# Kernel optimization log

Hardware: AMD Instinct MI355X
Metric: run time of the kernel (lower is better)

## Reference

```python
import jax, jax.numpy as jnp
import numpy as np

EPS = 1e-5

def _sparse_conv(x, nbr, W):
    # x: [N, Cin], nbr: [N, K] indices into rows of x, W: [K, Cin, Cout]
    # Minkowski-style kernel-map conv: gather neighbor feats, contract per offset.
    return jnp.einsum('nkc,kcd->nd', x[nbr], W)

def _bn(x, gamma, beta):
    # BatchNorm over all points (training-mode, biased variance)
    mu = x.mean(axis=0)
    var = x.var(axis=0)
    return (x - mu) * jax.lax.rsqrt(var + EPS) * gamma + beta

def setup_inputs() -> dict:
    key = jax.random.key(0)
    ks = jax.random.split(key, 6)
    N, K, Cin, Cout = 100000, 27, 64, 128
    x = jax.random.normal(ks[0], (N, Cin), dtype=jnp.float32)
    nbr = jax.random.randint(ks[1], (N, K), 0, N, dtype=jnp.int64)
    W1 = jax.random.normal(ks[2], (K, Cin, Cout), dtype=jnp.float32) / np.sqrt(K * Cin)
    W2 = jax.random.normal(ks[3], (K, Cout, Cout), dtype=jnp.float32) / np.sqrt(K * Cout)
    Wd = jax.random.normal(ks[4], (Cin, Cout), dtype=jnp.float32) / np.sqrt(Cin)
    ones = jnp.ones((Cout,), jnp.float32)
    zeros = jnp.zeros((Cout,), jnp.float32)
    return {"x": x, "nbr": nbr, "W1": W1, "g1": ones, "b1": zeros,
            "W2": W2, "g2": ones, "b2": zeros, "Wd": Wd, "gd": ones, "bd": zeros}

def reference(x, nbr, W1, g1, b1, W2, g2, b2, Wd, gd, bd):
    h = jax.nn.relu(_bn(_sparse_conv(x, nbr, W1), g1, b1))
    h = jax.nn.relu(_bn(_sparse_conv(h, nbr, W2), g2, b2))
    # downsample branch (input_nc != output_nc): 1x1 sparse conv == matmul, + BN
    res = _bn(x @ Wd, gd, bd)
    return h + res
```

## Files before the change

### kernel.cpp

```cpp
#include <hip/hip_runtime.h>
#include <hip/hip_bf16.h>

typedef unsigned short u16;
typedef unsigned int   u32;

#define COUT 128
#define KNB  27

typedef __attribute__((ext_vector_type(8))) __bf16 bf16x8;
typedef __attribute__((ext_vector_type(4))) float  f32x4;

__device__ float g_sum[2][128], g_sq[2][128];
__device__ float g_colsum[64], g_G[4096];
__device__ float g_sc[3][128], g_sh[3][128];
__device__ int   g_f32;
__device__ int   g_i64;
__device__ __attribute__((aligned(16))) u16 g_W1t[KNB * 128 * 64];
__device__ __attribute__((aligned(16))) u16 g_W2t[KNB * 128 * 128];

__device__ __forceinline__ float b2f(u32 u) {
    union { float f; u32 i; } v; v.i = u << 16; return v.f;
}
__device__ __forceinline__ u16 f2b(float f) {
    union { float f; u32 i; } v; v.f = f;
    u32 r = v.i + 0x7fffu + ((v.i >> 16) & 1u);
    return (u16)(r >> 16);
}
__device__ __forceinline__ float ldf(const void* p, int i, bool f32) {
    return f32 ? ((const float*)p)[i] : b2f((u32)((const u16*)p)[i]);
}

__device__ __forceinline__ void gld16(const void* g, void* l) {
    __builtin_amdgcn_global_load_lds(
        (const __attribute__((address_space(1))) u32*)g,
        (__attribute__((address_space(3))) u32*)l, 16, 0, 0);
}

__device__ __forceinline__ void lds_sync() {
    asm volatile("s_waitcnt lgkmcnt(0)" ::: "memory");
    __builtin_amdgcn_s_barrier();
    asm volatile("" ::: "memory");
}

__global__ void probe_zero_kernel(const u16* __restrict__ g1w, const int* __restrict__ nbr)
{
    int t = threadIdx.x;
    if (t == 0) {
        g_f32 = (g1w[0] == 0) ? 1 : 0;
        g_i64 = ((nbr[1] | nbr[3] | nbr[5] | nbr[7]) == 0) ? 1 : 0;
    }
    for (int i = t; i < 128; i += 256) {
        g_sum[0][i] = 0.f; g_sq[0][i] = 0.f;
        g_sum[1][i] = 0.f; g_sq[1][i] = 0.f;
    }
    for (int i = t; i < 64; i += 256) g_colsum[i] = 0.f;
    for (int i = t; i < 4096; i += 256) g_G[i] = 0.f;
}

__global__ void convert_w_kernel(const void* __restrict__ W1, const void* __restrict__ W2,
                                 const void* __restrict__ x, u16* __restrict__ xb, int N)
{
    const bool f32 = (g_f32 != 0);
    const int total1 = KNB * 64 * 128;
    const int total2 = KNB * 128 * 128;
    const int stride = gridDim.x * 256;
    for (int e = blockIdx.x * 256 + threadIdx.x; e < total1 + total2; e += stride) {
        if (e < total1) {
            int k = e / (64 * 128), r = e % (64 * 128);
            int c = r / 128, d = r % 128;
            g_W1t[(k * 128 + d) * 64 + c] = f2b(ldf(W1, e, f32));
        } else {
            int e2 = e - total1;
            int k = e2 / (128 * 128), r = e2 % (128 * 128);
            int c = r / 128, d = r % 128;
            g_W2t[(k * 128 + d) * 128 + c] = f2b(ldf(W2, e2, f32));
        }
    }
    const int totalx4 = (N * 64) / 4;
    for (int e = blockIdx.x * 256 + threadIdx.x; e < totalx4; e += stride) {
        if (f32) {
            float4 v = ((const float4*)x)[e];
            ushort4 r;
            r.x = f2b(v.x); r.y = f2b(v.y); r.z = f2b(v.z); r.w = f2b(v.w);
            ((ushort4*)xb)[e] = r;
        } else {
            ((uint2*)xb)[e] = ((const uint2*)x)[e];
        }
    }
}

__global__ __launch_bounds__(256)
void bn_relu_kernel(u16* __restrict__ tmp, int N)
{
    const int t  = threadIdx.x;
    const int c0 = (t & 15) * 8;
    float sc[8], sh[8];
#pragma unroll
    for (int j = 0; j < 8; ++j) { sc[j] = g_sc[0][c0 + j]; sh[j] = g_sh[0][c0 + j]; }
    const int total = N * (COUT / 8);
    for (int e = blockIdx.x * 256 + t; e < total; e += gridDim.x * 256) {
        uint4 u = ((const uint4*)tmp)[e];
        float v[8] = { b2f(u.x & 0xffffu), b2f(u.x >> 16),
                       b2f(u.y & 0xffffu), b2f(u.y >> 16),
                       b2f(u.z & 0xffffu), b2f(u.z >> 16),
                       b2f(u.w & 0xffffu), b2f(u.w >> 16) };
#pragma unroll
        for (int j = 0; j < 8; ++j) v[j] = fmaxf(fmaf(v[j], sc[j], sh[j]), 0.f);
        uint4 o;
        o.x = (u32)f2b(v[0]) | ((u32)f2b(v[1]) << 16);
        o.y = (u32)f2b(v[2]) | ((u32)f2b(v[3]) << 16);
        o.z = (u32)f2b(v[4]) | ((u32)f2b(v[5]) << 16);
        o.w = (u32)f2b(v[6]) | ((u32)f2b(v[7]) << 16);
        ((uint4*)tmp)[e] = o;
    }
}

template<int CIN, bool OUTF32, int WSEL, int SSEL>
__global__ __launch_bounds__(256, 2)
void spconv_mfma(const u16* __restrict__ src, const int* __restrict__ nbr,
                 void* __restrict__ outv, int N)
{
    constexpr int NCHUNK = CIN / 64;
    constexpr int STEPS  = KNB * NCHUNK;
    constexpr int OFF_ODD = (NCHUNK == 2) ? 64 : 0;
    const u16* __restrict__ Wt = (WSEL == 1) ? g_W1t : g_W2t;

    __shared__ __attribute__((aligned(16))) u16 As[2 * 8192];
    __shared__ __attribute__((aligned(16))) u16 Bs[2 * 8192];

    const int t    = threadIdx.x;
    const int lane = t & 63;
    const int w    = t >> 6;
    const int m    = lane & 15;
    const int q4   = lane >> 4;
    const int s_st = w >> 1;
    const int par  = w & 1;
    const int wm   = w >> 1;
    const int wn   = w & 1;
    const int n0   = blockIdx.x * 128;
    const int coff = (s_st * 4 + q4) * 8;
    const int kst  = (g_i64 != 0) ? 2 : 1;

    u32 nb0[4];
#pragma unroll
    for (int i = 0; i < 4; ++i) {
        int gr  = n0 + (2 * i + par) * 16 + m;
        int grc = (gr < N) ? gr : (N - 1);
        nb0[i] = (u32)grc * (u32)(KNB * kst);
    }

    f32x4 acc[4][4];
#pragma unroll
    for (int a = 0; a < 4; ++a)
#pragma unroll
        for (int b = 0; b < 4; ++b) acc[a][b] = (f32x4){0.f, 0.f, 0.f, 0.f};

    int idxE[4], idxO[4];

#define STEP_K(S)  ((NCHUNK == 2) ? ((S) >> 1) : (S))
#define LOAD_IDX(DST, K) do { \
    int kk_ = (K) < KNB ? (K) : (KNB - 1); \
    _Pragma("unroll") \
    for (int i_ = 0; i_ < 4; ++i_) \
        DST[i_] = nbr[nb0[i_] + (u32)kk_ * (u32)kst]; \
} while (0)

#define ISSUE_STEP(BUFO, IDX, K, C0N) do { \
    _Pragma("unroll") \
    for (int i_ = 0; i_ < 4; ++i_) { \
        const int tile_ = 2 * i_ + par; \
        u32 rw_ = (u32)(IDX)[i_]; if (rw_ >= (u32)N) rw_ = 0; \
        gld16(src + (size_t)rw_ * CIN + (C0N) + coff, \
              &As[(BUFO) + (tile_ * 2 + s_st) * 512]); \
        gld16(Wt + ((size_t)(K) * 128 + tile_ * 16 + m) * CIN + (C0N) + coff, \
              &Bs[(BUFO) + (tile_ * 2 + s_st) * 512]); \
    } \
} while (0)

#define MFMA_PHASE(LOFS) do { \
    __builtin_amdgcn_s_setprio(1); \
    _Pragma("unroll") \
    for (int s2_ = 0; s2_ < 2; ++s2_) { \
        bf16x8 afr_[4]; \
        _Pragma("unroll") \
        for (int mt_ = 0; mt_ < 4; ++mt_) \
            afr_[mt_] = *(const bf16x8*)&As[(LOFS) + (((wm * 4 + mt_) * 2 + s2_) * 512) + lane * 8]; \
        _Pragma("unroll") \
        for (int nt_ = 0; nt_ < 4; ++nt_) { \
            bf16x8 bfr_ = *(const bf16x8*)&Bs[(LOFS) + (((wn * 4 + nt_) * 2 + s2_) * 512) + lane * 8]; \
            _Pragma("unroll") \
            for (int mt_ = 0; mt_ < 4; ++mt_) \
                acc[mt_][nt_] = __builtin_amdgcn_mfma_f32_16x16x32_bf16( \
                    afr_[mt_], bfr_, acc[mt_][nt_], 0, 0, 0); \
        } \
    } \
    __builtin_amdgcn_s_setprio(0); \
} while (0)

    LOAD_IDX(idxE, 0);
    LOAD_IDX(idxO, STEP_K(1));
    ISSUE_STEP(0, idxE, 0, 0);
    LOAD_IDX(idxE, STEP_K(2));

#pragma clang loop unroll(disable)
    for (int s = 0; s < STEPS; s += 2) {
        lds_sync();
        if (s + 1 < STEPS) {
            ISSUE_STEP(8192, idxO, STEP_K(s + 1), OFF_ODD);
            LOAD_IDX(idxO, STEP_K(s + 3));
            asm volatile("s_waitcnt vmcnt(16)" ::: "memory");
        } else {
            asm volatile("s_waitcnt vmcnt(0)" ::: "memory");
        }
        __builtin_amdgcn_s_barrier();
        asm volatile("" ::: "memory");
        MFMA_PHASE(0);

        if (s + 1 < STEPS) {
            lds_sync();
            if (s + 2 < STEPS) {
                ISSUE_STEP(0, idxE, STEP_K(s + 2), 0);
                LOAD_IDX(idxE, STEP_K(s + 4));
                asm volatile("s_waitcnt vmcnt(16)" ::: "memory");
            } else {
                asm volatile("s_waitcnt vmcnt(0)" ::: "memory");
            }
            __builtin_amdgcn_s_barrier();
            asm volatile("" ::: "memory");
            MFMA_PHASE(8192);
        }
    }

    const int qq = lane >> 4, nn = lane & 15;
#pragma unroll
    for (int mt = 0; mt < 4; ++mt) {
#pragma unroll
        for (int r4 = 0; r4 < 4; ++r4) {
            int gr = n0 + (wm * 4 + mt) * 16 + qq * 4 + r4;
            if (gr < N) {
#pragma unroll
                for (int nt = 0; nt < 4; ++nt) {
                    float val = acc[mt][nt][r4];
                    size_t off = (size_t)gr * COUT + (wn * 4 + nt) * 16 + nn;
                    if constexpr (OUTF32) ((float*)outv)[off] = val;
                    else                  ((u16*)outv)[off]   = f2b(val);
                }
            }
        }
    }

    if constexpr (SSEL >= 0) {
        float sS[4], sQ[4];
#pragma unroll
        for (int nt = 0; nt < 4; ++nt) { sS[nt] = 0.f; sQ[nt] = 0.f; }
#pragma unroll
        for (int mt = 0; mt < 4; ++mt) {
#pragma unroll
            for (int r4 = 0; r4 < 4; ++r4) {
                int gr = n0 + (wm * 4 + mt) * 16 + qq * 4 + r4;
                bool ok = (gr < N);
#pragma unroll
                for (int nt = 0; nt < 4; ++nt) {
                    float v = ok ? acc[mt][nt][r4] : 0.f;
                    sS[nt] += v;
                    sQ[nt] = fmaf(v, v, sQ[nt]);
                }
            }
        }
#pragma unroll
        for (int nt = 0; nt < 4; ++nt) {
            sS[nt] += __shfl_xor(sS[nt], 16);
            sS[nt] += __shfl_xor(sS[nt], 32);
            sQ[nt] += __shfl_xor(sQ[nt], 16);
            sQ[nt] += __shfl_xor(sQ[nt], 32);
        }
        lds_sync();
        float* red = (float*)As;
        if (lane < 16) {
#pragma unroll
            for (int nt = 0; nt < 4; ++nt) {
                red[w * 64 + nt * 16 + lane]       = sS[nt];
                red[256 + w * 64 + nt * 16 + lane] = sQ[nt];
            }
        }
        lds_sync();
        if (t < 128) {
            int hi = t >> 6, lo = t & 63;
            float S = red[hi * 64 + lo] + red[(hi + 2) * 64 + lo];
            float Q = red[256 + hi * 64 + lo] + red[256 + (hi + 2) * 64 + lo];
            atomicAdd(&g_sum[SSEL][t], S);
            atomicAdd(&g_sq[SSEL][t],  Q);
        }
    }
#undef STEP_K
#undef LOAD_IDX
#undef ISSUE_STEP
#undef MFMA_PHASE
}

template<int SEL>
__global__ void finalize_kernel(const void* __restrict__ g, const void* __restrict__ b,
                                float invN)
{
    const bool f32 = (g_f32 != 0);
    int c = threadIdx.x;
    float mu  = g_sum[SEL][c] * invN;
    float var = fmaxf(g_sq[SEL][c] * invN - mu * mu, 0.f);
    float rs  = rsqrtf(var + 1e-5f);
    float sc  = rs * ldf(g, c, f32);
    g_sc[SEL][c] = sc;
    g_sh[SEL][c] = ldf(b, c, f32) - mu * sc;
}

__global__ __launch_bounds__(256)
void xstats_kernel(const void* __restrict__ xv, int N)
{
    __shared__ float xs[16 * 64];
    const bool f32 = (g_f32 != 0);
    const int t  = threadIdx.x;
    const int c  = t >> 2;
    const int cb = (t & 3) * 16;
    float acc[16];
#pragma unroll
    for (int j = 0; j < 16; ++j) acc[j] = 0.f;
    float cs = 0.f;

    for (int r0 = blockIdx.x * 16; r0 < N; r0 += gridDim.x * 16) {
        __syncthreads();
        {
            int e = t * 4;
            int rr = e >> 6, qq = e & 63;
            int row = r0 + rr;
            size_t off = (size_t)min(row, N - 1) * 64 + qq;
            bool ok = (row < N);
            float v0, v1, v2, v3;
            if (f32) {
                float4 vv = *(const float4*)((const float*)xv + off);
                v0 = vv.x; v1 = vv.y; v2 = vv.z; v3 = vv.w;
            } else {
                uint2 u = *(const uint2*)((const u16*)xv + off);
                v0 = b2f(u.x & 0xffffu); v1 = b2f(u.x >> 16);
                v2 = b2f(u.y & 0xffffu); v3 = b2f(u.y >> 16);
            }
            xs[e + 0] = ok ? v0 : 0.f;
            xs[e + 1] = ok ? v1 : 0.f;
            xs[e + 2] = ok ? v2 : 0.f;
            xs[e + 3] = ok ? v3 : 0.f;
        }
        __syncthreads();
#pragma unroll
        for (int rr = 0; rr < 16; ++rr) {
            float a = xs[rr * 64 + c];
#pragma unroll
            for (int j = 0; j < 16; ++j)
                acc[j] = fmaf(a, xs[rr * 64 + cb + j], acc[j]);
        }
        if (t < 64) {
#pragma unroll
            for (int rr = 0; rr < 16; ++rr) cs += xs[rr * 64 + t];
        }
    }
#pragma unroll
    for (int j = 0; j < 16; ++j) atomicAdd(&g_G[c * 64 + cb + j], acc[j]);
    if (t < 64) atomicAdd(&g_colsum[t], cs);
}

__global__ __launch_bounds__(128)
void finalize_d_kernel(const void* __restrict__ Wd, const void* __restrict__ gd,
                       const void* __restrict__ bd, float invN)
{
    __shared__ float Gs[64 * 64];
    const bool f32 = (g_f32 != 0);
    const int t = threadIdx.x;
    for (int e = t; e < 4096; e += 128) Gs[e] = g_G[e];
    __syncthreads();
    float w[64];
#pragma unroll
    for (int c = 0; c < 64; ++c) w[c] = ldf(Wd, c * 128 + t, f32);
    float s = 0.f, q = 0.f;
    for (int c = 0; c < 64; ++c) {
        float inner = 0.f;
#pragma unroll 8
        for (int cc = 0; cc < 64; ++cc) inner = fmaf(Gs[c * 64 + cc], w[cc], inner);
        q = fmaf(w[c], inner, q);
        s = fmaf(g_colsum[c], w[c], s);
    }
    float mu  = s * invN;
    float var = fmaxf(q * invN - mu * mu, 0.f);
    float rs  = rsqrtf(var + 1e-5f);
    float sc  = rs * ldf(gd, t, f32);
    g_sc[2][t] = sc;
    g_sh[2][t] = ldf(bd, t, f32) - mu * sc;
}

__global__ __launch_bounds__(256)
void finish_dense_kernel(const void* __restrict__ xv, const void* __restrict__ Wdv,
                         float* __restrict__ out, int N)
{
    __shared__ float Xs[64 * 68];
    __shared__ float Ws[64 * COUT];
    const bool f32 = (g_f32 != 0);
    const int t  = threadIdx.x;
    const int tx = t & 31;
    const int ty = t >> 5;
    const int n0 = blockIdx.x * 64;
    const int valid = min(64, N - n0);

    for (int e = t; e < 64 * 16; e += 256) {
        int mm = e >> 4;
        int qq = (e & 15) << 2;
        size_t off = (size_t)min(n0 + mm, N - 1) * 64 + qq;
        float v0, v1, v2, v3;
        if (f32) {
            float4 vv = *(const float4*)((const float*)xv + off);
            v0 = vv.x; v1 = vv.y; v2 = vv.z; v3 = vv.w;
        } else {
            uint2 u = *(const uint2*)((const u16*)xv + off);
            v0 = b2f(u.x & 0xffffu); v1 = b2f(u.x >> 16);
            v2 = b2f(u.y & 0xffffu); v3 = b2f(u.y >> 16);
        }
        *(float4*)&Xs[mm * 68 + qq] = make_float4(v0, v1, v2, v3);
    }
    if (f32) {
        const float* Wp = (const float*)Wdv;
        for (int e = t; e < (64 * COUT) / 8; e += 256) {
            int l = e << 3;
            float4 a = *(const float4*)(Wp + l);
            float4 b = *(const float4*)(Wp + l + 4);
            float* dst = &Ws[l];
            dst[0]=a.x; dst[1]=a.y; dst[2]=a.z; dst[3]=a.w;
            dst[4]=b.x; dst[5]=b.y; dst[6]=b.z; dst[7]=b.w;
        }
    } else {
        const u16* Wp = (const u16*)Wdv;
        for (int e = t; e < (64 * COUT) / 8; e += 256) {
            int l = e << 3;
            uint4 u = *(const uint4*)(Wp + l);
            float* dst = &Ws[l];
            dst[0] = b2f(u.x & 0xffffu); dst[1] = b2f(u.x >> 16);
            dst[2] = b2f(u.y & 0xffffu); dst[3] = b2f(u.y >> 16);
            dst[4] = b2f(u.z & 0xffffu); dst[5] = b2f(u.z >> 16);
            dst[6] = b2f(u.w & 0xffffu); dst[7] = b2f(u.w >> 16);
        }
    }
    __syncthreads();

    float acc[8][4];
#pragma unroll
    for (int mm = 0; mm < 8; ++mm)
#pragma unroll
        for (int j = 0; j < 4; ++j) acc[mm][j] = 0.f;

#pragma unroll 2
    for (int c = 0; c < 64; ++c) {
        float4 wv = *(const float4*)&Ws[c * COUT + tx * 4];
#pragma unroll
        for (int mm = 0; mm < 8; ++mm) {
            float a = Xs[(ty * 8 + mm) * 68 + c];
            acc[mm][0] = fmaf(a, wv.x, acc[mm][0]);
            acc[mm][1] = fmaf(a, wv.y, acc[mm][1]);
            acc[mm][2] = fmaf(a, wv.z, acc[mm][2]);
            acc[mm][3] = fmaf(a, wv.w, acc[mm][3]);
        }
    }

    const int d = tx * 4;
    float s2r[4] = {g_sc[1][d], g_sc[1][d+1], g_sc[1][d+2], g_sc[1][d+3]};
    float h2r[4] = {g_sh[1][d], g_sh[1][d+1], g_sh[1][d+2], g_sh[1][d+3]};
    float sdr[4] = {g_sc[2][d], g_sc[2][d+1], g_sc[2][d+2], g_sc[2][d+3]};
    float hdr[4] = {g_sh[2][d], g_sh[2][d+1], g_sh[2][d+2], g_sh[2][d+3]};
#pragma unroll
    for (int mm = 0; mm < 8; ++mm) {
        int rr = ty * 8 + mm;
        if (rr < valid) {
            float* p = out + (size_t)(n0 + rr) * COUT + d;
            float4 raw = *(float4*)p;
            float o0 = fmaxf(fmaf(raw.x, s2r[0], h2r[0]), 0.f) + fmaf(acc[mm][0], sdr[0], hdr[0]);
            float o1 = fmaxf(fmaf(raw.y, s2r[1], h2r[1]), 0.f) + fmaf(acc[mm][1], sdr[1], hdr[1]);
            float o2 = fmaxf(fmaf(raw.z, s2r[2], h2r[2]), 0.f) + fmaf(acc[mm][2], sdr[2], hdr[2]);
            float o3 = fmaxf(fmaf(raw.w, s2r[3], h2r[3]), 0.f) + fmaf(acc[mm][3], sdr[3], hdr[3]);
            *(float4*)p = make_float4(o0, o1, o2, o3);
        }
    }
}

extern "C" void kernel_launch(void* const* d_in, const int* in_sizes, int n_in,
                              void* d_out, int out_size, void* d_ws, size_t ws_size,
                              hipStream_t stream)
{
    const void* x   = d_in[0];
    const int*  nbr = (const int*)d_in[1];
    const void* W1  = d_in[2];
    const void* g1  = d_in[3];
    const void* b1  = d_in[4];
    const void* W2  = d_in[5];
    const void* g2  = d_in[6];
    const void* b2  = d_in[7];
    const void* Wd  = d_in[8];
    const void* gd  = d_in[9];
    const void* bd  = d_in[10];
    float* out = (float*)d_out;

    const int N = in_sizes[0] / 64;
    u16* tmp = (u16*)d_ws;
    u16* xb  = (u16*)d_out;

    const int nbm = (N + 127) / 128;
    const int nbf = (N + 63) / 64;
    const float invN = 1.f / (float)N;

    hipLaunchKernelGGL(probe_zero_kernel, dim3(1), dim3(256), 0, stream,
                       (const u16*)g1, nbr);
    hipLaunchKernelGGL(convert_w_kernel, dim3(1024), dim3(256), 0, stream,
                       W1, W2, x, xb, N);
    hipLaunchKernelGGL((spconv_mfma<64, false, 1, 0>), dim3(nbm), dim3(256), 0, stream,
                       xb, nbr, tmp, N);
    hipLaunchKernelGGL((finalize_kernel<0>), dim3(1), dim3(128), 0, stream, g1, b1, invN);
    hipLaunchKernelGGL(bn_relu_kernel, dim3(2048), dim3(256), 0, stream, tmp, N);
    hipLaunchKernelGGL((spconv_mfma<128, true, 2, 1>), dim3(nbm), dim3(256), 0, stream,
                       tmp, nbr, out, N);
    hipLaunchKernelGGL((finalize_kernel<1>), dim3(1), dim3(128), 0, stream, g2, b2, invN);
    hipLaunchKernelGGL(xstats_kernel, dim3(256), dim3(256), 0, stream, x, N);
    hipLaunchKernelGGL(finalize_d_kernel, dim3(1), dim3(128), 0, stream, Wd, gd, bd, invN);
    hipLaunchKernelGGL(finish_dense_kernel, dim3(nbf), dim3(256), 0, stream,
                       x, Wd, out, N);
}
```

Before: 811.7 us.

## Halve K-chunk to 32 channels to cut LDS and raise occupancy to four blocks

The sparse-conv MFMA kernel now stages 32-channel chunks per step instead of 64, halving the A/B LDS double buffers. Launch bounds rise to four blocks per CU, and each step issues fewer gathers with adjusted vmcnt waits. The aim is more resident waves to hide the latency of random neighbor gathers. In exchange there are twice as many pipeline steps and barriers, each with less MFMA work, and a tighter register budget that could spill.

After: 827.7 us. Within noise of the previous version (+2.0%).

```diff
diff --git a/kernel.cpp b/kernel.cpp
--- a/kernel.cpp
+++ b/kernel.cpp
@@ -116,35 +116,31 @@
 }
 
 template<int CIN, bool OUTF32, int WSEL, int SSEL>
-__global__ __launch_bounds__(256, 2)
+__global__ __launch_bounds__(256, 4)
 void spconv_mfma(const u16* __restrict__ src, const int* __restrict__ nbr,
                  void* __restrict__ outv, int N)
 {
-    constexpr int NCHUNK = CIN / 64;
-    constexpr int STEPS  = KNB * NCHUNK;
-    constexpr int OFF_ODD = (NCHUNK == 2) ? 64 : 0;
+    constexpr int CHUNKS = CIN / 32;
+    constexpr int STEPS  = KNB * CHUNKS;
     const u16* __restrict__ Wt = (WSEL == 1) ? g_W1t : g_W2t;
 
-    __shared__ __attribute__((aligned(16))) u16 As[2 * 8192];
-    __shared__ __attribute__((aligned(16))) u16 Bs[2 * 8192];
+    __shared__ __attribute__((aligned(16))) u16 As[2 * 4096];
+    __shared__ __attribute__((aligned(16))) u16 Bs[2 * 4096];
 
     const int t    = threadIdx.x;
     const int lane = t & 63;
     const int w    = t >> 6;
     const int m    = lane & 15;
     const int q4   = lane >> 4;
-    const int s_st = w >> 1;
-    const int par  = w & 1;
     const int wm   = w >> 1;
     const int wn   = w & 1;
     const int n0   = blockIdx.x * 128;
-    const int coff = (s_st * 4 + q4) * 8;
     const int kst  = (g_i64 != 0) ? 2 : 1;
 
-    u32 nb0[4];
-#pragma unroll
-    for (int i = 0; i < 4; ++i) {
-        int gr  = n0 + (2 * i + par) * 16 + m;
+    u32 nb0[2];
+#pragma unroll
+    for (int i = 0; i < 2; ++i) {
+        int gr  = n0 + (w + 4 * i) * 16 + m;
         int grc = (gr < N) ? gr : (N - 1);
         nb0[i] = (u32)grc * (u32)(KNB * kst);
     }
@@ -155,44 +151,41 @@
 #pragma unroll
         for (int b = 0; b < 4; ++b) acc[a][b] = (f32x4){0.f, 0.f, 0.f, 0.f};
 
-    int idxE[4], idxO[4];
-
-#define STEP_K(S)  ((NCHUNK == 2) ? ((S) >> 1) : (S))
+    int idxE[2], idxO[2];
+
+#define STEP_K(S)  ((S) / CHUNKS)
 #define LOAD_IDX(DST, K) do { \
     int kk_ = (K) < KNB ? (K) : (KNB - 1); \
+    DST[0] = nbr[nb0[0] + (u32)kk_ * (u32)kst]; \
+    DST[1] = nbr[nb0[1] + (u32)kk_ * (u32)kst]; \
+} while (0)
+
+#define ISSUE_STEP(BUFO, IDX, K, S) do { \
+    const int cb_ = ((S) & (CHUNKS - 1)) * 32; \
     _Pragma("unroll") \
-    for (int i_ = 0; i_ < 4; ++i_) \
-        DST[i_] = nbr[nb0[i_] + (u32)kk_ * (u32)kst]; \
-} while (0)
-
-#define ISSUE_STEP(BUFO, IDX, K, C0N) do { \
-    _Pragma("unroll") \
-    for (int i_ = 0; i_ < 4; ++i_) { \
-        const int tile_ = 2 * i_ + par; \
+    for (int i_ = 0; i_ < 2; ++i_) { \
+        const int mt_ = w + 4 * i_; \
         u32 rw_ = (u32)(IDX)[i_]; if (rw_ >= (u32)N) rw_ = 0; \
-        gld16(src + (size_t)rw_ * CIN + (C0N) + coff, \
-              &As[(BUFO) + (tile_ * 2 + s_st) * 512]); \
-        gld16(Wt + ((size_t)(K) * 128 + tile_ * 16 + m) * CIN + (C0N) + coff, \
-              &Bs[(BUFO) + (tile_ * 2 + s_st) * 512]); \
+        gld16(src + (size_t)rw_ * CIN + cb_ + q4 * 8, \
+              &As[(BUFO) + mt_ * 512]); \
+        gld16(Wt + ((size_t)(K) * 128 + mt_ * 16 + m) * CIN + cb_ + q4 * 8, \
+              &Bs[(BUFO) + mt_ * 512]); \
     } \
 } while (0)
 
 #define MFMA_PHASE(LOFS) do { \
     __builtin_amdgcn_s_setprio(1); \
+    bf16x8 afr_[4]; \
     _Pragma("unroll") \
-    for (int s2_ = 0; s2_ < 2; ++s2_) { \
-        bf16x8 afr_[4]; \
+    for (int mt_ = 0; mt_ < 4; ++mt_) \
+        afr_[mt_] = *(const bf16x8*)&As[(LOFS) + (wm * 4 + mt_) * 512 + lane * 8]; \
+    _Pragma("unroll") \
+    for (int nt_ = 0; nt_ < 4; ++nt_) { \
+        bf16x8 bfr_ = *(const bf16x8*)&Bs[(LOFS) + (wn * 4 + nt_) * 512 + lane * 8]; \
         _Pragma("unroll") \
         for (int mt_ = 0; mt_ < 4; ++mt_) \
-            afr_[mt_] = *(const bf16x8*)&As[(LOFS) + (((wm * 4 + mt_) * 2 + s2_) * 512) + lane * 8]; \
-        _Pragma("unroll") \
-        for (int nt_ = 0; nt_ < 4; ++nt_) { \
-            bf16x8 bfr_ = *(const bf16x8*)&Bs[(LOFS) + (((wn * 4 + nt_) * 2 + s2_) * 512) + lane * 8]; \
-            _Pragma("unroll") \
-            for (int mt_ = 0; mt_ < 4; ++mt_) \
-                acc[mt_][nt_] = __builtin_amdgcn_mfma_f32_16x16x32_bf16( \
-                    afr_[mt_], bfr_, acc[mt_][nt_], 0, 0, 0); \
-        } \
+            acc[mt_][nt_] = __builtin_amdgcn_mfma_f32_16x16x32_bf16( \
+                afr_[mt_], bfr_, acc[mt_][nt_], 0, 0, 0); \
     } \
     __builtin_amdgcn_s_setprio(0); \
 } while (0)
@@ -205,30 +198,24 @@
 #pragma clang loop unroll(disable)
     for (int s = 0; s < STEPS; s += 2) {
         lds_sync();
-        if (s + 1 < STEPS) {
-            ISSUE_STEP(8192, idxO, STEP_K(s + 1), OFF_ODD);
-            LOAD_IDX(idxO, STEP_K(s + 3));
-            asm volatile("s_waitcnt vmcnt(16)" ::: "memory");
-        } else {
-            asm volatile("s_waitcnt vmcnt(0)" ::: "memory");
-        }
+        ISSUE_STEP(4096, idxO, STEP_K(s + 1), s + 1);
+        LOAD_IDX(idxO, STEP_K(s + 3));
+        asm volatile("s_waitcnt vmcnt(6)" ::: "memory");
         __builtin_amdgcn_s_barrier();
         asm volatile("" ::: "memory");
         MFMA_PHASE(0);
 
-        if (s + 1 < STEPS) {
-            lds_sync();
-            if (s + 2 < STEPS) {
-                ISSUE_STEP(0, idxE, STEP_K(s + 2), 0);
-                LOAD_IDX(idxE, STEP_K(s + 4));
-                asm volatile("s_waitcnt vmcnt(16)" ::: "memory");
-            } else {
-                asm volatile("s_waitcnt vmcnt(0)" ::: "memory");
-            }
-            __builtin_amdgcn_s_barrier();
-            asm volatile("" ::: "memory");
-            MFMA_PHASE(8192);
-        }
+        lds_sync();
+        if (s + 2 < STEPS) {
+            ISSUE_STEP(0, idxE, STEP_K(s + 2), s + 2);
+            LOAD_IDX(idxE, STEP_K(s + 4));
+            asm volatile("s_waitcnt vmcnt(6)" ::: "memory");
+        } else {
+            asm volatile("s_waitcnt vmcnt(0)" ::: "memory");
+        }
+        __builtin_amdgcn_s_barrier();
+        asm volatile("" ::: "memory");
+        MFMA_PHASE(4096);
     }
 
     const int qq = lane >> 4, nn = lane & 15;
```

## Stage neighbor indices in LDS and gather full-row swizzled A tiles

Applied to the files above, without the earlier changes.

Each block now preloads its 128x27 neighbor index table into shared memory once, so the per-step index loads come from LDS instead of global memory. The A-tile gather is remapped so 8 consecutive lanes fetch one contiguous 128-byte row segment, stored with an XOR swizzle, and the MFMA fragment reads use precomputed swizzled offsets. The vmcnt wait threshold drops because global loads per step no longer include index fetches, and an odd-step tail is handled explicitly. This adds shared-memory usage (about 14 KB) and a prologue sync, which could reduce occupancy.

Result: faster. 704.5 us (-13.2%).

```diff
diff --git a/kernel.cpp b/kernel.cpp
--- a/kernel.cpp
+++ b/kernel.cpp
@@ -120,33 +120,43 @@
 void spconv_mfma(const u16* __restrict__ src, const int* __restrict__ nbr,
                  void* __restrict__ outv, int N)
 {
-    constexpr int NCHUNK = CIN / 64;
-    constexpr int STEPS  = KNB * NCHUNK;
-    constexpr int OFF_ODD = (NCHUNK == 2) ? 64 : 0;
+    constexpr int CHUNKS  = CIN / 64;
+    constexpr int STEPS   = KNB * CHUNKS;
+    constexpr int MAINEND = STEPS & ~1;
     const u16* __restrict__ Wt = (WSEL == 1) ? g_W1t : g_W2t;
 
     __shared__ __attribute__((aligned(16))) u16 As[2 * 8192];
     __shared__ __attribute__((aligned(16))) u16 Bs[2 * 8192];
+    __shared__ u32 nbrl[128 * 28];
 
     const int t    = threadIdx.x;
     const int lane = t & 63;
     const int w    = t >> 6;
-    const int m    = lane & 15;
-    const int q4   = lane >> 4;
-    const int s_st = w >> 1;
-    const int par  = w & 1;
+    const int mh   = lane & 15;
+    const int qh   = lane >> 4;
     const int wm   = w >> 1;
     const int wn   = w & 1;
     const int n0   = blockIdx.x * 128;
-    const int coff = (s_st * 4 + q4) * 8;
     const int kst  = (g_i64 != 0) ? 2 : 1;
 
-    u32 nb0[4];
-#pragma unroll
-    for (int i = 0; i < 4; ++i) {
-        int gr  = n0 + (2 * i + par) * 16 + m;
+    const int r8   = lane >> 3;
+    const int gaw  = ((lane & 7) ^ (r8 & 7)) * 8;
+
+    for (int e = t; e < 128 * KNB; e += 256) {
+        int row = e / KNB, kk = e - row * KNB;
+        int gr  = n0 + row;
         int grc = (gr < N) ? gr : (N - 1);
-        nb0[i] = (u32)grc * (u32)(KNB * kst);
+        nbrl[row * 28 + kk] = (u32)nbr[(size_t)grc * (KNB * kst) + (size_t)kk * kst];
+    }
+    __syncthreads();
+
+    int aoff[2][4];
+#pragma unroll
+    for (int mt = 0; mt < 4; ++mt) {
+        int rr   = wm * 64 + mt * 16 + mh;
+        int base = (rr >> 3) * 512 + (rr & 7) * 64;
+        aoff[0][mt] = base + ((qh       ^ (mh & 7)) * 8);
+        aoff[1][mt] = base + (((4 + qh) ^ (mh & 7)) * 8);
     }
 
     f32x4 acc[4][4];
@@ -155,93 +165,101 @@
 #pragma unroll
         for (int b = 0; b < 4; ++b) acc[a][b] = (f32x4){0.f, 0.f, 0.f, 0.f};
 
-    int idxE[4], idxO[4];
-
-#define STEP_K(S)  ((NCHUNK == 2) ? ((S) >> 1) : (S))
-#define LOAD_IDX(DST, K) do { \
-    int kk_ = (K) < KNB ? (K) : (KNB - 1); \
+    int idx0[4], idxE[4], idxO[4];
+
+#define KOF(S)  ((CHUNKS == 2) ? ((S) >> 1) : (S))
+#define CB(S)   ((CHUNKS == 2) ? (((S) & 1) * 64) : 0)
+
+#define IDXRD(DST, S) do { \
+    int kk_ = KOF(S); if (kk_ > KNB - 1) kk_ = KNB - 1; \
     _Pragma("unroll") \
-    for (int i_ = 0; i_ < 4; ++i_) \
-        DST[i_] = nbr[nb0[i_] + (u32)kk_ * (u32)kst]; \
+    for (int j_ = 0; j_ < 4; ++j_) \
+        DST[j_] = (int)nbrl[(w * 32 + j_ * 8 + r8) * 28 + kk_]; \
 } while (0)
 
-#define ISSUE_STEP(BUFO, IDX, K, C0N) do { \
+#define ISSUE_STEP(BUFO, IDX, S) do { \
+    const int cb_ = CB(S); const int k_ = KOF(S); \
     _Pragma("unroll") \
-    for (int i_ = 0; i_ < 4; ++i_) { \
-        const int tile_ = 2 * i_ + par; \
-        u32 rw_ = (u32)(IDX)[i_]; if (rw_ >= (u32)N) rw_ = 0; \
-        gld16(src + (size_t)rw_ * CIN + (C0N) + coff, \
-              &As[(BUFO) + (tile_ * 2 + s_st) * 512]); \
-        gld16(Wt + ((size_t)(K) * 128 + tile_ * 16 + m) * CIN + (C0N) + coff, \
-              &Bs[(BUFO) + (tile_ * 2 + s_st) * 512]); \
+    for (int j_ = 0; j_ < 4; ++j_) { \
+        u32 r_ = (u32)(IDX)[j_]; if (r_ >= (u32)N) r_ = 0; \
+        gld16(src + (size_t)r_ * CIN + cb_ + gaw, \
+              &As[(BUFO) + (w * 4 + j_) * 512]); \
+    } \
+    _Pragma("unroll") \
+    for (int j_ = 0; j_ < 4; ++j_) { \
+        const int sx_ = w * 4 + j_;                     \
+        gld16(Wt + ((size_t)k_ * 128 + (sx_ >> 1) * 16 + mh) * CIN + cb_ \
+                 + (sx_ & 1) * 32 + qh * 8, \
+              &Bs[(BUFO) + sx_ * 512]); \
     } \
 } while (0)
 
-#define MFMA_PHASE(LOFS) do { \
+#define MFMA_PHASE(BUFO) do { \
     __builtin_amdgcn_s_setprio(1); \
     _Pragma("unroll") \
-    for (int s2_ = 0; s2_ < 2; ++s2_) { \
-        bf16x8 afr_[4]; \
+    for (int ks_ = 0; ks_ < 2; ++ks_) { \
+        bf16x8 af_[4]; \
         _Pragma("unroll") \
         for (int mt_ = 0; mt_ < 4; ++mt_) \
-            afr_[mt_] = *(const bf16x8*)&As[(LOFS) + (((wm * 4 + mt_) * 2 + s2_) * 512) + lane * 8]; \
+            af_[mt_] = *(const bf16x8*)&As[(BUFO) + aoff[ks_][mt_]]; \
         _Pragma("unroll") \
         for (int nt_ = 0; nt_ < 4; ++nt_) { \
-            bf16x8 bfr_ = *(const bf16x8*)&Bs[(LOFS) + (((wn * 4 + nt_) * 2 + s2_) * 512) + lane * 8]; \
+            bf16x8 bf_ = *(const bf16x8*)&Bs[(BUFO) + \
+                (((wn * 4 + nt_) * 2 + ks_) * 512) + lane * 8]; \
             _Pragma("unroll") \
             for (int mt_ = 0; mt_ < 4; ++mt_) \
                 acc[mt_][nt_] = __builtin_amdgcn_mfma_f32_16x16x32_bf16( \
-                    afr_[mt_], bfr_, acc[mt_][nt_], 0, 0, 0); \
+                    af_[mt_], bf_, acc[mt_][nt_], 0, 0, 0); \
         } \
     } \
     __builtin_amdgcn_s_setprio(0); \
 } while (0)
 
-    LOAD_IDX(idxE, 0);
-    LOAD_IDX(idxO, STEP_K(1));
-    ISSUE_STEP(0, idxE, 0, 0);
-    LOAD_IDX(idxE, STEP_K(2));
+    IDXRD(idx0, 0);
+    IDXRD(idxO, 1);
+    ISSUE_STEP(0, idx0, 0);
+    IDXRD(idxE, 2);
 
 #pragma clang loop unroll(disable)
-    for (int s = 0; s < STEPS; s += 2) {
+    for (int s = 0; s < MAINEND; s += 2) {
         lds_sync();
-        if (s + 1 < STEPS) {
-            ISSUE_STEP(8192, idxO, STEP_K(s + 1), OFF_ODD);
-            LOAD_IDX(idxO, STEP_K(s + 3));
-            asm volatile("s_waitcnt vmcnt(16)" ::: "memory");
-        } else {
-            asm volatile("s_waitcnt vmcnt(0)" ::: "memory");
-        }
+        ISSUE_STEP(8192, idxO, s + 1);
+        IDXRD(idxO, s + 3);
+        asm volatile("s_waitcnt vmcnt(8)" ::: "memory");
         __builtin_amdgcn_s_barrier();
         asm volatile("" ::: "memory");
         MFMA_PHASE(0);
 
-        if (s + 1 < STEPS) {
-            lds_sync();
-            if (s + 2 < STEPS) {
-                ISSUE_STEP(0, idxE, STEP_K(s + 2), 0);
-                LOAD_IDX(idxE, STEP_K(s + 4));
-                asm volatile("s_waitcnt vmcnt(16)" ::: "memory");
-            } else {
-                asm volatile("s_waitcnt vmcnt(0)" ::: "memory");
-            }
-            __builtin_amdgcn_s_barrier();
-            asm volatile("" ::: "memory");
-            MFMA_PHASE(8192);
-        }
-    }
-
-    const int qq = lane >> 4, nn = lane & 15;
+        lds_sync();
+        if (s + 2 < STEPS) {
+            ISSUE_STEP(0, idxE, s + 2);
+            IDXRD(idxE, s + 4);
+            asm volatile("s_waitcnt vmcnt(8)" ::: "memory");
+        } else {
+            asm volatile("s_waitcnt vmcnt(0)" ::: "memory");
+        }
+        __builtin_amdgcn_s_barrier();
+        asm volatile("" ::: "memory");
+        MFMA_PHASE(8192);
+    }
+    if constexpr (STEPS & 1) {
+        lds_sync();
+        asm volatile("s_waitcnt vmcnt(0)" ::: "memory");
+        __builtin_amdgcn_s_barrier();
+        asm volatile("" ::: "memory");
+        MFMA_PHASE(0);
+    }
+
 #pragma unroll
     for (int mt = 0; mt < 4; ++mt) {
 #pragma unroll
         for (int r4 = 0; r4 < 4; ++r4) {
-            int gr = n0 + (wm * 4 + mt) * 16 + qq * 4 + r4;
+            int gr = n0 + (wm * 4 + mt) * 16 + qh * 4 + r4;
             if (gr < N) {
 #pragma unroll
                 for (int nt = 0; nt < 4; ++nt) {
                     float val = acc[mt][nt][r4];
-                    size_t off = (size_t)gr * COUT + (wn * 4 + nt) * 16 + nn;
+                    size_t off = (size_t)gr * COUT + (wn * 4 + nt) * 16 + mh;
                     if constexpr (OUTF32) ((float*)outv)[off] = val;
                     else                  ((u16*)outv)[off]   = f2b(val);
                 }
@@ -257,7 +275,7 @@
         for (int mt = 0; mt < 4; ++mt) {
 #pragma unroll
             for (int r4 = 0; r4 < 4; ++r4) {
-                int gr = n0 + (wm * 4 + mt) * 16 + qq * 4 + r4;
+                int gr = n0 + (wm * 4 + mt) * 16 + qh * 4 + r4;
                 bool ok = (gr < N);
 #pragma unroll
                 for (int nt = 0; nt < 4; ++nt) {
@@ -292,8 +310,9 @@
             atomicAdd(&g_sq[SSEL][t],  Q);
         }
     }
-#undef STEP_K
-#undef LOAD_IDX
+#undef KOF
+#undef CB
+#undef IDXRD
 #undef ISSUE_STEP
 #undef MFMA_PHASE
 }
```
